# Performance work log

Hardware: AMD Instinct MI355X
Metric: run time of the kernel (lower is better)

## Reference

```python
import jax, jax.numpy as jnp
import numpy as np

L, H, E, V, BS = 12, 12, 768, 50257, 1024
HS = E // H
EPS = 1e-5


def _ln(x, w, b):
    m = jnp.mean(x, axis=-1, keepdims=True)
    v = jnp.mean(jnp.square(x - m), axis=-1, keepdims=True)
    return (x - m) * jax.lax.rsqrt(v + EPS) * w + b


def setup_inputs() -> dict:
    key = jax.random.key(0)
    ks = jax.random.split(key, 16)
    s = 0.02
    inp = {
        "idx": jax.random.randint(ks[0], (2, 1024), 0, V),
        "wte": jax.random.normal(ks[1], (V, E), jnp.float32) * s,
        "wpe": jax.random.normal(ks[2], (BS, E), jnp.float32) * s,
        "ln1_w": jnp.ones((L, E), jnp.float32),
        "ln1_b": jnp.zeros((L, E), jnp.float32),
        "attn_w": jax.random.normal(ks[3], (L, E, 3 * E), jnp.float32) * s,
        "attn_b": jnp.zeros((L, 3 * E), jnp.float32),
        "proj_w": jax.random.normal(ks[4], (L, E, E), jnp.float32) * s,
        "proj_b": jnp.zeros((L, E), jnp.float32),
        "ln2_w": jnp.ones((L, E), jnp.float32),
        "ln2_b": jnp.zeros((L, E), jnp.float32),
        "fc_w": jax.random.normal(ks[5], (L, E, 4 * E), jnp.float32) * s,
        "fc_b": jnp.zeros((L, 4 * E), jnp.float32),
        "fcp_w": jax.random.normal(ks[6], (L, 4 * E, E), jnp.float32) * s,
        "fcp_b": jnp.zeros((L, E), jnp.float32),
        "lnf_w": jnp.ones((E,), jnp.float32),
        "lnf_b": jnp.zeros((E,), jnp.float32),
    }
    return inp


def _gpt_forward(idx, wte, wpe, ln1_w, ln1_b, attn_w, attn_b, proj_w, proj_b,
                 ln2_w, ln2_b, fc_w, fc_b, fcp_w, fcp_b, lnf_w, lnf_b):
    B, T = idx.shape
    x = wte[idx] + wpe[:T]  # [B,T,E]
    causal = jnp.tril(jnp.ones((T, T), bool))
    scale = 1.0 / np.sqrt(HS)

    def block(x, p):
        (l1w, l1b, aw, ab, pw, pb, l2w, l2b, fw, fb, pww, pwb) = p
        qkv = _ln(x, l1w, l1b) @ aw + ab  # [B,T,3E]
        q, k, v = jnp.split(qkv, 3, axis=-1)
        q = q.reshape(B, T, H, HS).transpose(0, 2, 1, 3)  # [B,H,T,hs]
        k = k.reshape(B, T, H, HS).transpose(0, 2, 1, 3)
        v = v.reshape(B, T, H, HS).transpose(0, 2, 1, 3)
        att = jnp.einsum('bhqd,bhkd->bhqk', q, k) * scale
        att = jnp.where(causal, att, -jnp.inf)
        att = jax.nn.softmax(att, axis=-1)
        y = jnp.einsum('bhqk,bhkd->bhqd', att, v)
        y = y.transpose(0, 2, 1, 3).reshape(B, T, E)
        x = x + y @ pw + pb
        h = jax.nn.gelu(_ln(x, l2w, l2b) @ fw + fb, approximate=False)
        x = x + h @ pww + pwb
        return x, None

    params = (ln1_w, ln1_b, attn_w, attn_b, proj_w, proj_b,
              ln2_w, ln2_b, fc_w, fc_b, fcp_w, fcp_b)
    x, _ = jax.lax.scan(block, x, params)
    x = _ln(x, lnf_w, lnf_b)
    return x @ wte.T  # tied lm_head, training-mode full logits [B,T,V]


def reference(idx, wte, wpe, ln1_w, ln1_b, attn_w, attn_b, proj_w, proj_b,
              ln2_w, ln2_b, fc_w, fc_b, fcp_w, fcp_b, lnf_w, lnf_b):
    return _gpt_forward(idx, wte, wpe, ln1_w, ln1_b, attn_w, attn_b, proj_w,
                        proj_b, ln2_w, ln2_b, fc_w, fc_b, fcp_w, fcp_b,
                        lnf_w, lnf_b)
```

## Files before the change

kernel.cpp:

```cpp
#include <hip/hip_runtime.h>
#include <hip/hip_bf16.h>


typedef __bf16 bf16x8 __attribute__((ext_vector_type(8)));
typedef float f32x4 __attribute__((ext_vector_type(4)));
typedef unsigned int u32x4 __attribute__((ext_vector_type(4)));
typedef unsigned short ushort_t;

__device__ inline unsigned short f2bf(float f) {
    unsigned int u = __float_as_uint(f);
    u += 0x7FFFu + ((u >> 16) & 1u);
    return (unsigned short)(u >> 16);
}
__device__ inline unsigned int pk2(float a, float b) {
    return (unsigned int)f2bf(a) | ((unsigned int)f2bf(b) << 16);
}
__device__ inline float gelu_f(float v) {
    return 0.5f * v * (1.0f + erff(v * 0.70710678118654752f));
}
__device__ inline void gld16(const ushort_t* g, ushort_t* l) {
    __builtin_amdgcn_global_load_lds(
        (const __attribute__((address_space(1))) void*)g,
        (__attribute__((address_space(3))) void*)l, 16, 0, 0);
}
__device__ inline void store_c(float* p, float v) { *p = v; }
__device__ inline void store_c(ushort_t* p, float v) { *p = f2bf(v); }

__device__ inline void ln_body(
    const float* __restrict__ in, const float* __restrict__ w,
    const float* __restrict__ b, ushort_t* __restrict__ out, int row) {
    const float* r = in + (size_t)row * 768;
    int tid = threadIdx.x;
    float v[3];
#pragma unroll
    for (int j = 0; j < 3; j++) v[j] = r[tid + j * 256];
    float s = v[0] + v[1] + v[2];
    __shared__ float sh1[4], sh2[4];
#pragma unroll
    for (int o = 32; o; o >>= 1) s += __shfl_down(s, o);
    if ((tid & 63) == 0) sh1[tid >> 6] = s;
    __syncthreads();
    float mean = (sh1[0] + sh1[1] + sh1[2] + sh1[3]) * (1.0f / 768.0f);
    float d0 = v[0] - mean, d1 = v[1] - mean, d2 = v[2] - mean;
    float sq = d0 * d0 + d1 * d1 + d2 * d2;
#pragma unroll
    for (int o = 32; o; o >>= 1) sq += __shfl_down(sq, o);
    if ((tid & 63) == 0) sh2[tid >> 6] = sq;
    __syncthreads();
    float var = (sh2[0] + sh2[1] + sh2[2] + sh2[3]) * (1.0f / 768.0f);
    float rstd = rsqrtf(var + 1e-5f);
#pragma unroll
    for (int j = 0; j < 3; j++) {
        int c = tid + j * 256;
        out[(size_t)row * 768 + c] = f2bf((v[j] - mean) * rstd * w[c] + b[c]);
    }
}

__global__ __launch_bounds__(256) void ln_kernel(
    const float* __restrict__ in, const float* __restrict__ w,
    const float* __restrict__ b, ushort_t* __restrict__ out) {
    ln_body(in, w, b, out, blockIdx.x);
}

__device__ inline void transpose_tile(
    const float* __restrict__ in, ushort_t* __restrict__ out,
    int N, int K, int n0, int k0) {
    __shared__ float tl[64][65];
    int tid = threadIdx.x;
    int r = tid >> 4, c = (tid & 15) * 4;
#pragma unroll
    for (int j = 0; j < 4; j++) {
        float4 v = *(const float4*)(in + (size_t)(k0 + r + j * 16) * N + n0 + c);
        tl[r + j * 16][c] = v.x; tl[r + j * 16][c + 1] = v.y;
        tl[r + j * 16][c + 2] = v.z; tl[r + j * 16][c + 3] = v.w;
    }
    __syncthreads();
    int nr = tid >> 2, kc = (tid & 3) * 16;
    unsigned int u[8];
#pragma unroll
    for (int j = 0; j < 8; j++)
        u[j] = pk2(tl[kc + 2 * j][nr], tl[kc + 2 * j + 1][nr]);
    u32x4 a = {u[0], u[1], u[2], u[3]}, b = {u[4], u[5], u[6], u[7]};
    ushort_t* op = out + (size_t)(n0 + nr) * K + k0 + kc;
    *(u32x4*)op = a;
    *(u32x4*)(op + 8) = b;
}

__device__ inline void transpose_dispatch(
    int t,
    const float* __restrict__ aw, const float* __restrict__ pw,
    const float* __restrict__ fw, const float* __restrict__ fpw,
    ushort_t* __restrict__ awT, ushort_t* __restrict__ pwT,
    ushort_t* __restrict__ fwT, ushort_t* __restrict__ fpwT) {
    if (t < 432)       transpose_tile(aw,  awT,  2304, 768, (t % 36) * 64, (t / 36) * 64);
    else if (t < 576)  { t -= 432;  transpose_tile(pw,  pwT,  768,  768, (t % 12) * 64, (t / 12) * 64); }
    else if (t < 1152) { t -= 576;  transpose_tile(fw,  fwT,  3072, 768, (t % 48) * 64, (t / 48) * 64); }
    else               { t -= 1152; transpose_tile(fpw, fpwT, 768, 3072, (t % 12) * 64, (t / 12) * 64); }
}

__global__ __launch_bounds__(256) void embed0_kernel(
    const int* __restrict__ idx, const float* __restrict__ wte,
    const float* __restrict__ wpe, float* __restrict__ x,
    const float* __restrict__ aw, const float* __restrict__ pw,
    const float* __restrict__ fw, const float* __restrict__ fpw,
    ushort_t* __restrict__ awT, ushort_t* __restrict__ pwT,
    ushort_t* __restrict__ fwT, ushort_t* __restrict__ fpwT) {
    int t = blockIdx.x;
    if (t < 2048) {
        int row = t, tt = row & 1023;
        int tok = idx[row];
        int tid = threadIdx.x;
#pragma unroll
        for (int j = 0; j < 3; j++) {
            int c = tid + j * 256;
            x[(size_t)row * 768 + c] = wte[(size_t)tok * 768 + c] + wpe[(size_t)tt * 768 + c];
        }
        return;
    }
    transpose_dispatch(t - 2048, aw, pw, fw, fpw, awT, pwT, fwT, fpwT);
}

__global__ __launch_bounds__(256) void lnfconv_kernel(
    const float* __restrict__ x, const float* __restrict__ lw,
    const float* __restrict__ lb, ushort_t* __restrict__ xn,
    const float* __restrict__ wte, ushort_t* __restrict__ wteb) {
    int t = blockIdx.x;
    if (t < 2048) { ln_body(x, lw, lb, xn, t); return; }
    const long long n8 = (50257LL * 768) / 8;
    long long i = (long long)(t - 2048) * 256 + threadIdx.x;
    long long stride = 4096LL * 256;
    for (; i < n8; i += stride) {
        const float4* s = (const float4*)(wte + i * 8);
        float4 a = s[0], b = s[1];
        u32x4 u = {pk2(a.x, a.y), pk2(a.z, a.w), pk2(b.x, b.y), pk2(b.z, b.w)};
        *(u32x4*)(wteb + i * 8) = u;
    }
}

__global__ __launch_bounds__(256) void attn_tr_kernel(
    const ushort_t* __restrict__ qkvb,
    const ushort_t* __restrict__ vt,
    ushort_t* __restrict__ y,
    const float* __restrict__ aw, const float* __restrict__ pw,
    const float* __restrict__ fw, const float* __restrict__ fpw,
    ushort_t* __restrict__ awT, ushort_t* __restrict__ pwT,
    ushort_t* __restrict__ fwT, ushort_t* __restrict__ fpwT) {
    if (blockIdx.x >= 192) {
        transpose_dispatch(blockIdx.x - 192, aw, pw, fw, fpw, awT, pwT, fwT, fpwT);
        return;
    }
    int bid = blockIdx.x;
    int qt = 7 - (bid & 7);
    int q0 = qt * 128;
    int z = bid >> 3;
    int b = z / 12, h = z % 12;

    __shared__ __align__(16) ushort_t Ks[64 * 64];
    __shared__ __align__(16) ushort_t Vs[64 * 64];
    __shared__ __align__(16) ushort_t Ps[4][32 * 72];

    int tid = threadIdx.x;
    int lane = tid & 63, w = tid >> 6;
    int fr = lane & 15;
    int g4 = lane >> 4;
    int kg = g4 * 8;

    const ushort_t* qbase = qkvb + (size_t)b * 1024 * 2304;
    bf16x8 qf[2][2];
#pragma unroll
    for (int m = 0; m < 2; m++)
#pragma unroll
        for (int ks = 0; ks < 2; ks++)
            qf[m][ks] = *(const bf16x8*)(qbase +
                (size_t)(q0 + w * 32 + m * 16 + fr) * 2304 + h * 64 + ks * 32 + kg);

    f32x4 oacc[2][4] = {};
    float mrow[2][4], lrow[2][4];
#pragma unroll
    for (int m = 0; m < 2; m++)
#pragma unroll
        for (int i = 0; i < 4; i++) { mrow[m][i] = -1e30f; lrow[m][i] = 0.f; }

    const ushort_t* vtb = vt + (size_t)z * 64 * 1024;
    int nkt = ((q0 + 127) >> 6) + 1;
    const float LOG2E = 1.4426950408889634f;
    const float sc = 0.125f;
    int swr = (fr & 7) << 3;

    for (int kt = 0; kt < nkt; kt++) {
        int k0 = kt << 6;
#pragma unroll
        for (int c2 = 0; c2 < 2; c2++) {
            int c = tid + c2 * 256;
            int row = c >> 3;
            int col8 = ((c & 7) << 3) ^ ((row & 7) << 3);
            gld16(qbase + (size_t)(k0 + row) * 2304 + 768 + h * 64 + col8, Ks + c * 8);
            gld16(vtb + (size_t)row * 1024 + k0 + col8, Vs + c * 8);
        }
        __syncthreads();
        bool active = (k0 <= q0 + w * 32 + 31);
        if (active) {
            f32x4 s[2][4] = {};
#pragma unroll
            for (int ks = 0; ks < 2; ks++) {
                int cc = (ks * 32 + kg) ^ swr;
                bf16x8 kf[4];
#pragma unroll
                for (int n = 0; n < 4; n++)
                    kf[n] = *(const bf16x8*)(Ks + (n * 16 + fr) * 64 + cc);
#pragma unroll
                for (int m = 0; m < 2; m++)
#pragma unroll
                    for (int n = 0; n < 4; n++)
                        s[m][n] = __builtin_amdgcn_mfma_f32_16x16x32_bf16(qf[m][ks], kf[n], s[m][n], 0, 0, 0);
            }
            float al[2][4];
#pragma unroll
            for (int m = 0; m < 2; m++) {
#pragma unroll
                for (int i = 0; i < 4; i++) {
                    int q = q0 + w * 32 + m * 16 + g4 * 4 + i;
                    float pm = -1e30f;
#pragma unroll
                    for (int n = 0; n < 4; n++) {
                        int kv = k0 + n * 16 + fr;
                        float v = (kv <= q) ? s[m][n][i] * sc : -1e30f;
                        s[m][n][i] = v;
                        pm = fmaxf(pm, v);
                    }
                    pm = fmaxf(pm, __shfl_xor(pm, 1));
                    pm = fmaxf(pm, __shfl_xor(pm, 2));
                    pm = fmaxf(pm, __shfl_xor(pm, 4));
                    pm = fmaxf(pm, __shfl_xor(pm, 8));
                    float mn = fmaxf(mrow[m][i], pm);
                    float alpha = __builtin_exp2f((mrow[m][i] - mn) * LOG2E);
                    mrow[m][i] = mn;
                    al[m][i] = alpha;
                    float ps = 0.f;
#pragma unroll
                    for (int n = 0; n < 4; n++) {
                        float pv = __builtin_exp2f((s[m][n][i] - mn) * LOG2E);
                        s[m][n][i] = pv;
                        ps += pv;
                    }
                    ps += __shfl_xor(ps, 1);
                    ps += __shfl_xor(ps, 2);
                    ps += __shfl_xor(ps, 4);
                    ps += __shfl_xor(ps, 8);
                    lrow[m][i] = lrow[m][i] * alpha + ps;
                }
            }
#pragma unroll
            for (int m = 0; m < 2; m++)
#pragma unroll
                for (int nd = 0; nd < 4; nd++)
#pragma unroll
                    for (int i = 0; i < 4; i++)
                        oacc[m][nd][i] *= al[m][i];
#pragma unroll
            for (int m = 0; m < 2; m++)
#pragma unroll
                for (int n = 0; n < 4; n++)
#pragma unroll
                    for (int i = 0; i < 4; i++)
                        Ps[w][(m * 16 + g4 * 4 + i) * 72 + n * 16 + fr] = f2bf(s[m][n][i]);
        }
        __syncthreads();
        if (active) {
#pragma unroll
            for (int ks = 0; ks < 2; ks++) {
                int cc = (ks * 32 + kg) ^ swr;
                bf16x8 pa[2], vf[4];
#pragma unroll
                for (int m = 0; m < 2; m++)
                    pa[m] = *(const bf16x8*)(&Ps[w][(m * 16 + fr) * 72 + ks * 32 + kg]);
#pragma unroll
                for (int nd = 0; nd < 4; nd++)
                    vf[nd] = *(const bf16x8*)(Vs + (nd * 16 + fr) * 64 + cc);
#pragma unroll
                for (int m = 0; m < 2; m++)
#pragma unroll
                    for (int nd = 0; nd < 4; nd++)
                        oacc[m][nd] = __builtin_amdgcn_mfma_f32_16x16x32_bf16(pa[m], vf[nd], oacc[m][nd], 0, 0, 0);
            }
        }
        __syncthreads();
    }
    ushort_t* yb = y + (size_t)b * 1024 * 768 + h * 64;
#pragma unroll
    for (int m = 0; m < 2; m++)
#pragma unroll
        for (int nd = 0; nd < 4; nd++)
#pragma unroll
            for (int i = 0; i < 4; i++) {
                int q = q0 + w * 32 + m * 16 + g4 * 4 + i;
                yb[(size_t)q * 768 + nd * 16 + fr] = f2bf(oacc[m][nd][i] / lrow[m][i]);
            }
}

template <int BM, int EPI, typename TC>
__global__ __launch_bounds__(256) void gemm2(
    const ushort_t* __restrict__ A, int lda,
    const ushort_t* __restrict__ B, int ldb,
    TC* __restrict__ C, int ldc,
    const float* __restrict__ bias, const float* __restrict__ R,
    ushort_t* __restrict__ VT,
    int M, int N, int K) {
    constexpr int MR = BM / 32;
    int brow = blockIdx.y * BM;
    int bcol = blockIdx.x * 128;

    __shared__ __align__(16) ushort_t As[BM * 64];
    __shared__ __align__(16) ushort_t Bs[128 * 64];
    __shared__ __align__(16) ushort_t Tr[EPI == 3 ? 128 * 80 : 1];

    int tid = threadIdx.x;
    int lane = tid & 63, wid = tid >> 6;
    int wr = (wid >> 1) * (BM / 2);
    int wc = (wid & 1) * 64;
    int fr = lane & 15;
    int g4 = lane >> 4;
    int kg = g4 * 8;
    int swr = (fr & 7) << 3;

    int colk = ((tid & 7) << 3) ^ (((tid >> 3) & 7) << 3);
    const ushort_t* Agr[MR];
    const ushort_t* Bgr[4];
#pragma unroll
    for (int rg = 0; rg < MR; rg++)
        Agr[rg] = A + (size_t)(brow + rg * 32 + (tid >> 3)) * lda + colk;
#pragma unroll
    for (int rg = 0; rg < 4; rg++) {
        int br = bcol + rg * 32 + (tid >> 3);
        if (br > N - 1) br = N - 1;
        Bgr[rg] = B + (size_t)br * ldb + colk;
    }
    ushort_t* Al = As + tid * 8;
    ushort_t* Bl = Bs + tid * 8;

    f32x4 acc[MR][4] = {};

    for (int k0 = 0; k0 < K; k0 += 64) {
#pragma unroll
        for (int rg = 0; rg < MR; rg++) gld16(Agr[rg] + k0, Al + rg * 2048);
#pragma unroll
        for (int rg = 0; rg < 4; rg++) gld16(Bgr[rg] + k0, Bl + rg * 2048);
        __syncthreads();
#pragma unroll
        for (int ks = 0; ks < 2; ks++) {
            int cc = (ks * 32 + kg) ^ swr;
            bf16x8 af[MR], bfv[4];
#pragma unroll
            for (int m = 0; m < MR; m++)
                af[m] = *(const bf16x8*)(As + (wr + m * 16 + fr) * 64 + cc);
#pragma unroll
            for (int n = 0; n < 4; n++)
                bfv[n] = *(const bf16x8*)(Bs + (wc + n * 16 + fr) * 64 + cc);
#pragma unroll
            for (int m = 0; m < MR; m++)
#pragma unroll
                for (int n = 0; n < 4; n++)
                    acc[m][n] = __builtin_amdgcn_mfma_f32_16x16x32_bf16(af[m], bfv[n], acc[m][n], 0, 0, 0);
        }
        __syncthreads();
    }

    int cr = g4 * 4;

    if constexpr (EPI == 3) {
        if (bcol >= 1536) {
#pragma unroll
            for (int m = 0; m < MR; m++) {
#pragma unroll
                for (int n = 0; n < 4; n++) {
                    int dl = wc + n * 16 + fr;
                    float bv = bias[bcol + dl];
#pragma unroll
                    for (int i = 0; i < 4; i++) {
                        int tl = wr + m * 16 + cr + i;
                        Tr[dl * 80 + tl] = f2bf(acc[m][n][i] + bv);
                    }
                }
            }
            __syncthreads();
            int bb = brow >> 10, t0g = brow & 1023;
            int dbase = bcol - 1536;
#pragma unroll
            for (int j = 0; j < 4; j++) {
                int lin = tid + j * 256;
                int dl = lin >> 3, t8 = (lin & 7) * 8;
                int dg = dbase + dl;
                int h2 = dg >> 6, dd = dg & 63;
                u32x4 v = *(const u32x4*)&Tr[dl * 80 + t8];
                *(u32x4*)(VT + ((size_t)(bb * 12 + h2) * 64 + dd) * 1024 + t0g + t8) = v;
            }
            return;
        }
    }

#pragma unroll
    for (int m = 0; m < MR; m++) {
#pragma unroll
        for (int n = 0; n < 4; n++) {
            int col = bcol + wc + n * 16 + fr;
            if (col < N) {
                float bv = bias ? bias[col] : 0.0f;
#pragma unroll
                for (int i = 0; i < 4; i++) {
                    int row = brow + wr + m * 16 + cr + i;
                    float v = acc[m][n][i] + bv;
                    if constexpr (EPI == 1) v = gelu_f(v);
                    if constexpr (EPI == 2) v += R[(size_t)row * ldc + col];
                    store_c(&C[(size_t)row * ldc + col], v);
                }
            }
        }
    }
}

__global__ __launch_bounds__(512, 1) void gemm256(
    const ushort_t* __restrict__ A, int lda,
    const ushort_t* __restrict__ B, int ldb,
    float* __restrict__ C, int ldc,
    int M, int N, int K) {
    int Rt = gridDim.x, P = gridDim.y;
    int wgid = blockIdx.x + Rt * blockIdx.y;
    int full = P >> 3;
    int thresh = full * 8 * Rt;
    int r, pp;
    if (wgid < thresh) {
        int g = wgid / (8 * Rt);
        int wi = wgid - g * (8 * Rt);
        r = wi >> 3;
        pp = g * 8 + (wi & 7);
    } else {
        int off = wgid - thresh;
        pp = full * 8 + off / Rt;
        r = off - (off / Rt) * Rt;
    }
    int brow = r * 256;
    int bcol = pp * 256;

    __shared__ __align__(16) ushort_t As[2][256 * 64];
    __shared__ __align__(16) ushort_t Bs[2][256 * 64];

    int tid = threadIdx.x;
    int lane = tid & 63, wid = tid >> 6;
    int wr = (wid >> 2) * 128;
    int wc = (wid & 3) * 64;
    int fr = lane & 15;
    int g4 = lane >> 4;
    int kg = g4 * 8;
    int swr = (fr & 7) << 3;

    int srow = tid >> 3;
    int scol = ((tid & 7) << 3) ^ ((srow & 7) << 3);
    const ushort_t* Ag[4];
    const ushort_t* Bg[4];
#pragma unroll
    for (int s = 0; s < 4; s++) {
        Ag[s] = A + (size_t)(brow + s * 64 + srow) * lda + scol;
        int br = bcol + s * 64 + srow;
        if (br > N - 1) br = N - 1;
        Bg[s] = B + (size_t)br * ldb + scol;
    }

    f32x4 acc[8][4] = {};
    int nt = K >> 6;

#pragma unroll
    for (int s = 0; s < 4; s++) {
        gld16(Ag[s], &As[0][s * 4096 + tid * 8]);
        gld16(Bg[s], &Bs[0][s * 4096 + tid * 8]);
    }

    for (int t = 0; t < nt; t++) {
        int cur = t & 1;
        if (t + 1 < nt) {
            int nxt = cur ^ 1;
            int k0 = (t + 1) << 6;
#pragma unroll
            for (int s = 0; s < 4; s++) {
                gld16(Ag[s] + k0, &As[nxt][s * 4096 + tid * 8]);
                gld16(Bg[s] + k0, &Bs[nxt][s * 4096 + tid * 8]);
            }
            asm volatile("s_waitcnt vmcnt(8)" ::: "memory");
        } else {
            asm volatile("s_waitcnt vmcnt(0)" ::: "memory");
        }
        __builtin_amdgcn_sched_barrier(0);
        __builtin_amdgcn_s_barrier();
        __builtin_amdgcn_sched_barrier(0);

        const ushort_t* Ab = &As[cur][0];
        const ushort_t* Bb = &Bs[cur][0];
#pragma unroll
        for (int ks = 0; ks < 2; ks++) {
            int cc = (ks * 32 + kg) ^ swr;
            bf16x8 af[8], bfv[4];
#pragma unroll
            for (int m = 0; m < 8; m++)
                af[m] = *(const bf16x8*)(Ab + (wr + m * 16 + fr) * 64 + cc);
#pragma unroll
            for (int n = 0; n < 4; n++)
                bfv[n] = *(const bf16x8*)(Bb + (wc + n * 16 + fr) * 64 + cc);
#pragma unroll
            for (int m = 0; m < 8; m++)
#pragma unroll
                for (int n = 0; n < 4; n++)
                    acc[m][n] = __builtin_amdgcn_mfma_f32_16x16x32_bf16(af[m], bfv[n], acc[m][n], 0, 0, 0);
        }
        asm volatile("s_waitcnt lgkmcnt(0)" ::: "memory");
        __builtin_amdgcn_sched_barrier(0);
        __builtin_amdgcn_s_barrier();
        __builtin_amdgcn_sched_barrier(0);
    }

    int cr = g4 * 4;
#pragma unroll
    for (int m = 0; m < 8; m++) {
#pragma unroll
        for (int n = 0; n < 4; n++) {
            int col = bcol + wc + n * 16 + fr;
            if (col < N) {
#pragma unroll
                for (int i = 0; i < 4; i++) {
                    int row = brow + wr + m * 16 + cr + i;
                    __builtin_nontemporal_store(acc[m][n][i], &C[(size_t)row * ldc + col]);
                }
            }
        }
    }
}

extern "C" void kernel_launch(void* const* d_in, const int* in_sizes, int n_in,
                              void* d_out, int out_size, void* d_ws, size_t ws_size,
                              hipStream_t stream) {
    const int*   idx    = (const int*)d_in[0];
    const float* wte    = (const float*)d_in[1];
    const float* wpe    = (const float*)d_in[2];
    const float* ln1_w  = (const float*)d_in[3];
    const float* ln1_b  = (const float*)d_in[4];
    const float* attn_w = (const float*)d_in[5];
    const float* attn_b = (const float*)d_in[6];
    const float* proj_w = (const float*)d_in[7];
    const float* proj_b = (const float*)d_in[8];
    const float* ln2_w  = (const float*)d_in[9];
    const float* ln2_b  = (const float*)d_in[10];
    const float* fc_w   = (const float*)d_in[11];
    const float* fc_b   = (const float*)d_in[12];
    const float* fcp_w  = (const float*)d_in[13];
    const float* fcp_b  = (const float*)d_in[14];
    const float* lnf_w  = (const float*)d_in[15];
    const float* lnf_b  = (const float*)d_in[16];
    float* out = (float*)d_out;

    const size_t S_AW = (size_t)2304 * 768, S_PW = (size_t)768 * 768;
    const size_t S_FW = (size_t)3072 * 768, S_FPW = (size_t)768 * 3072;

    char* p = (char*)d_ws;
    float*    x    = (float*)p;    p += (size_t)2048 * 768 * 4;
    ushort_t* xn   = (ushort_t*)p; p += (size_t)2048 * 768 * 2;
    ushort_t* qkvb = (ushort_t*)p; p += (size_t)2048 * 2304 * 2;
    ushort_t* y    = (ushort_t*)p; p += (size_t)2048 * 768 * 2;
    ushort_t* h    = (ushort_t*)p; p += (size_t)2048 * 3072 * 2;
    ushort_t* vt   = (ushort_t*)p; p += (size_t)24 * 64 * 1024 * 2;
    ushort_t* wteb = (ushort_t*)p; p += (size_t)50257 * 768 * 2;
    ushort_t* awT[2], *pwT[2], *fwT[2], *fpwT[2];
    for (int i = 0; i < 2; i++) {
        awT[i]  = (ushort_t*)p; p += S_AW * 2;
        pwT[i]  = (ushort_t*)p; p += S_PW * 2;
        fwT[i]  = (ushort_t*)p; p += S_FW * 2;
        fpwT[i] = (ushort_t*)p; p += S_FPW * 2;
    }

    embed0_kernel<<<3776, 256, 0, stream>>>(
        idx, wte, wpe, x,
        attn_w, proj_w, fc_w, fcp_w, awT[0], pwT[0], fwT[0], fpwT[0]);

    for (int l = 0; l < 12; l++) {
        int cb = l & 1, nb = cb ^ 1;
        ln_kernel<<<2048, 256, 0, stream>>>(x, ln1_w + l * 768, ln1_b + l * 768, xn);
        gemm2<64, 3, ushort_t><<<dim3(18, 32), 256, 0, stream>>>(
            xn, 768, awT[cb], 768, qkvb, 2304,
            attn_b + l * 2304, nullptr, vt, 2048, 2304, 768);
        int nblk = (l < 11) ? 1920 : 192;
        attn_tr_kernel<<<nblk, 256, 0, stream>>>(
            qkvb, vt, y,
            attn_w + (size_t)(l + 1) * S_AW, proj_w + (size_t)(l + 1) * S_PW,
            fc_w + (size_t)(l + 1) * S_FW, fcp_w + (size_t)(l + 1) * S_FPW,
            awT[nb], pwT[nb], fwT[nb], fpwT[nb]);
        gemm2<64, 2, float><<<dim3(6, 32), 256, 0, stream>>>(
            y, 768, pwT[cb], 768, x, 768,
            proj_b + l * 768, x, nullptr, 2048, 768, 768);
        ln_kernel<<<2048, 256, 0, stream>>>(x, ln2_w + l * 768, ln2_b + l * 768, xn);
        gemm2<64, 1, ushort_t><<<dim3(24, 32), 256, 0, stream>>>(
            xn, 768, fwT[cb], 768, h, 3072,
            fc_b + l * 3072, nullptr, nullptr, 2048, 3072, 768);
        gemm2<64, 2, float><<<dim3(6, 32), 256, 0, stream>>>(
            h, 3072, fpwT[cb], 3072, x, 768,
            fcp_b + l * 768, x, nullptr, 2048, 768, 3072);
    }

    lnfconv_kernel<<<6144, 256, 0, stream>>>(x, lnf_w, lnf_b, xn, wte, wteb);
    gemm256<<<dim3(8, 197), 512, 0, stream>>>(
        xn, 768, wteb, 768, out, 50257, 2048, 50257, 768);
}
```

Before: 2.468 ms.

## Process two row tiles per LM-head block and overlap first tile's stores with second's compute

Each LM-head GEMM workgroup now computes two consecutive 256-row tiles sharing the same B (wte) column tile, halving the grid in the row dimension. The first tile's accumulators are written out row-fragment by row-fragment during the first eight K-steps of the second tile, so the output stores overlap with the loads and MFMAs. Nontemporal stores are replaced with plain stores. This doubles the accumulator registers held live, which may lower occupancy or cause spills, and the grid of half as many blocks may leave CUs less balanced.

```diff
diff --git a/kernel.cpp b/kernel.cpp
--- a/kernel.cpp
+++ b/kernel.cpp
@@ -438,7 +438,7 @@
         pp = full * 8 + off / Rt;
         r = off - (off / Rt) * Rt;
     }
-    int brow = r * 256;
+    int brow0 = r * 512;
     int bcol = pp * 256;
 
     __shared__ __align__(16) ushort_t As[2][256 * 64];
@@ -455,68 +455,140 @@
 
     int srow = tid >> 3;
     int scol = ((tid & 7) << 3) ^ ((srow & 7) << 3);
-    const ushort_t* Ag[4];
     const ushort_t* Bg[4];
 #pragma unroll
     for (int s = 0; s < 4; s++) {
-        Ag[s] = A + (size_t)(brow + s * 64 + srow) * lda + scol;
         int br = bcol + s * 64 + srow;
         if (br > N - 1) br = N - 1;
         Bg[s] = B + (size_t)br * ldb + scol;
     }
-
-    f32x4 acc[8][4] = {};
     int nt = K >> 6;
-
-#pragma unroll
-    for (int s = 0; s < 4; s++) {
-        gld16(Ag[s], &As[0][s * 4096 + tid * 8]);
-        gld16(Bg[s], &Bs[0][s * 4096 + tid * 8]);
-    }
-
-    for (int t = 0; t < nt; t++) {
-        int cur = t & 1;
-        if (t + 1 < nt) {
-            int nxt = cur ^ 1;
-            int k0 = (t + 1) << 6;
-#pragma unroll
-            for (int s = 0; s < 4; s++) {
-                gld16(Ag[s] + k0, &As[nxt][s * 4096 + tid * 8]);
-                gld16(Bg[s] + k0, &Bs[nxt][s * 4096 + tid * 8]);
-            }
-            asm volatile("s_waitcnt vmcnt(8)" ::: "memory");
-        } else {
-            asm volatile("s_waitcnt vmcnt(0)" ::: "memory");
-        }
-        __builtin_amdgcn_sched_barrier(0);
-        __builtin_amdgcn_s_barrier();
-        __builtin_amdgcn_sched_barrier(0);
-
-        const ushort_t* Ab = &As[cur][0];
-        const ushort_t* Bb = &Bs[cur][0];
-#pragma unroll
-        for (int ks = 0; ks < 2; ks++) {
-            int cc = (ks * 32 + kg) ^ swr;
-            bf16x8 af[8], bfv[4];
-#pragma unroll
-            for (int m = 0; m < 8; m++)
-                af[m] = *(const bf16x8*)(Ab + (wr + m * 16 + fr) * 64 + cc);
-#pragma unroll
-            for (int n = 0; n < 4; n++)
-                bfv[n] = *(const bf16x8*)(Bb + (wc + n * 16 + fr) * 64 + cc);
-#pragma unroll
-            for (int m = 0; m < 8; m++)
+    int cr = g4 * 4;
+
+    f32x4 acc0[8][4] = {};
+    {
+        const ushort_t* Ag[4];
+#pragma unroll
+        for (int s = 0; s < 4; s++)
+            Ag[s] = A + (size_t)(brow0 + s * 64 + srow) * lda + scol;
+#pragma unroll
+        for (int s = 0; s < 4; s++) {
+            gld16(Ag[s], &As[0][s * 4096 + tid * 8]);
+            gld16(Bg[s], &Bs[0][s * 4096 + tid * 8]);
+        }
+        for (int t = 0; t < nt; t++) {
+            int cur = t & 1;
+            if (t + 1 < nt) {
+                int nxt = cur ^ 1;
+                int k0 = (t + 1) << 6;
+#pragma unroll
+                for (int s = 0; s < 4; s++) {
+                    gld16(Ag[s] + k0, &As[nxt][s * 4096 + tid * 8]);
+                    gld16(Bg[s] + k0, &Bs[nxt][s * 4096 + tid * 8]);
+                }
+                asm volatile("s_waitcnt vmcnt(8)" ::: "memory");
+            } else {
+                asm volatile("s_waitcnt vmcnt(0)" ::: "memory");
+            }
+            __builtin_amdgcn_sched_barrier(0);
+            __builtin_amdgcn_s_barrier();
+            __builtin_amdgcn_sched_barrier(0);
+            const ushort_t* Ab = &As[cur][0];
+            const ushort_t* Bb = &Bs[cur][0];
+#pragma unroll
+            for (int ks = 0; ks < 2; ks++) {
+                int cc = (ks * 32 + kg) ^ swr;
+                bf16x8 af[8], bfv[4];
+#pragma unroll
+                for (int m = 0; m < 8; m++)
+                    af[m] = *(const bf16x8*)(Ab + (wr + m * 16 + fr) * 64 + cc);
 #pragma unroll
                 for (int n = 0; n < 4; n++)
-                    acc[m][n] = __builtin_amdgcn_mfma_f32_16x16x32_bf16(af[m], bfv[n], acc[m][n], 0, 0, 0);
-        }
-        asm volatile("s_waitcnt lgkmcnt(0)" ::: "memory");
-        __builtin_amdgcn_sched_barrier(0);
-        __builtin_amdgcn_s_barrier();
-        __builtin_amdgcn_sched_barrier(0);
-    }
-
-    int cr = g4 * 4;
+                    bfv[n] = *(const bf16x8*)(Bb + (wc + n * 16 + fr) * 64 + cc);
+#pragma unroll
+                for (int m = 0; m < 8; m++)
+#pragma unroll
+                    for (int n = 0; n < 4; n++)
+                        acc0[m][n] = __builtin_amdgcn_mfma_f32_16x16x32_bf16(af[m], bfv[n], acc0[m][n], 0, 0, 0);
+            }
+            asm volatile("s_waitcnt lgkmcnt(0)" ::: "memory");
+            __builtin_amdgcn_sched_barrier(0);
+            __builtin_amdgcn_s_barrier();
+            __builtin_amdgcn_sched_barrier(0);
+        }
+    }
+
+    int brow1 = brow0 + 256;
+    f32x4 acc1[8][4] = {};
+    {
+        const ushort_t* Ag[4];
+#pragma unroll
+        for (int s = 0; s < 4; s++)
+            Ag[s] = A + (size_t)(brow1 + s * 64 + srow) * lda + scol;
+#pragma unroll
+        for (int s = 0; s < 4; s++) {
+            gld16(Ag[s], &As[0][s * 4096 + tid * 8]);
+            gld16(Bg[s], &Bs[0][s * 4096 + tid * 8]);
+        }
+        for (int t = 0; t < nt; t++) {
+            int cur = t & 1;
+            bool st = (t < 8);
+            if (st) {
+                int m = t;
+#pragma unroll
+                for (int n = 0; n < 4; n++) {
+                    int col = bcol + wc + n * 16 + fr;
+                    if (col < N) {
+#pragma unroll
+                        for (int i = 0; i < 4; i++) {
+                            int row = brow0 + wr + m * 16 + cr + i;
+                            C[(size_t)row * ldc + col] = acc0[m][n][i];
+                        }
+                    }
+                }
+                __builtin_amdgcn_sched_barrier(0);
+            }
+            if (t + 1 < nt) {
+                int nxt = cur ^ 1;
+                int k0 = (t + 1) << 6;
+#pragma unroll
+                for (int s = 0; s < 4; s++) {
+                    gld16(Ag[s] + k0, &As[nxt][s * 4096 + tid * 8]);
+                    gld16(Bg[s] + k0, &Bs[nxt][s * 4096 + tid * 8]);
+                }
+                if (st) asm volatile("s_waitcnt vmcnt(24)" ::: "memory");
+                else    asm volatile("s_waitcnt vmcnt(8)" ::: "memory");
+            } else {
+                asm volatile("s_waitcnt vmcnt(0)" ::: "memory");
+            }
+            __builtin_amdgcn_sched_barrier(0);
+            __builtin_amdgcn_s_barrier();
+            __builtin_amdgcn_sched_barrier(0);
+            const ushort_t* Ab = &As[cur][0];
+            const ushort_t* Bb = &Bs[cur][0];
+#pragma unroll
+            for (int ks = 0; ks < 2; ks++) {
+                int cc = (ks * 32 + kg) ^ swr;
+                bf16x8 af[8], bfv[4];
+#pragma unroll
+                for (int m = 0; m < 8; m++)
+                    af[m] = *(const bf16x8*)(Ab + (wr + m * 16 + fr) * 64 + cc);
+#pragma unroll
+                for (int n = 0; n < 4; n++)
+                    bfv[n] = *(const bf16x8*)(Bb + (wc + n * 16 + fr) * 64 + cc);
+#pragma unroll
+                for (int m = 0; m < 8; m++)
+#pragma unroll
+                    for (int n = 0; n < 4; n++)
+                        acc1[m][n] = __builtin_amdgcn_mfma_f32_16x16x32_bf16(af[m], bfv[n], acc1[m][n], 0, 0, 0);
+            }
+            asm volatile("s_waitcnt lgkmcnt(0)" ::: "memory");
+            __builtin_amdgcn_sched_barrier(0);
+            __builtin_amdgcn_s_barrier();
+            __builtin_amdgcn_sched_barrier(0);
+        }
+    }
+
 #pragma unroll
     for (int m = 0; m < 8; m++) {
 #pragma unroll
@@ -525,8 +597,8 @@
             if (col < N) {
 #pragma unroll
                 for (int i = 0; i < 4; i++) {
-                    int row = brow + wr + m * 16 + cr + i;
-                    __builtin_nontemporal_store(acc[m][n][i], &C[(size_t)row * ldc + col]);
+                    int row = brow1 + wr + m * 16 + cr + i;
+                    C[(size_t)row * ldc + col] = acc1[m][n][i];
                 }
             }
         }
@@ -603,6 +675,6 @@
     }
 
     lnfconv_kernel<<<6144, 256, 0, stream>>>(x, lnf_w, lnf_b, xn, wte, wteb);
-    gemm256<<<dim3(8, 197), 512, 0, stream>>>(
+    gemm256<<<dim3(4, 197), 512, 0, stream>>>(
         xn, 768, wteb, 768, out, 50257, 2048, 50257, 768);
 }
```

Result: faster. 2.379 ms (-3.6%).
